# Kernel optimization log

Hardware: AMD Instinct MI355X
Metric: run time of the kernel (lower is better)

The kernel has to match this reference:

```python
import jax, jax.numpy as jnp
import numpy as np

EPS = 1e-6

def _quant_per_token(x):
    # dynamic per-token symmetric int8 quantization (simulated in float)
    s = jnp.max(jnp.abs(x), axis=-1, keepdims=True) / 127.0  # [T,1]
    q = jnp.clip(jnp.round(x / s), -127.0, 127.0)
    return q, s

def _quant_weight(W):
    # per-output-channel symmetric int8 weight quantization (W: [out,in])
    s = jnp.max(jnp.abs(W), axis=1, keepdims=True) / 127.0  # [out,1]
    q = jnp.round(W / s)
    return q, s

def _w8a8(qx, sx, W, b):
    # int8xint8 GEMM with per-token act scale and per-channel weight scale, fp out
    qw, sw = _quant_weight(W)
    return (qx @ qw.T) * (sx * sw.T) + b

def _rmsnorm_bias(x, w, b, eps=EPS):
    # RMSNormGeneral: x * rsqrt(mean(x^2)+eps) * w + b (no mean subtraction)
    var = jnp.mean(x * x, axis=-1, keepdims=True)
    return x * jax.lax.rsqrt(var + eps) * w + b

def setup_inputs() -> dict:
    key = jax.random.key(0)
    ks = jax.random.split(key, 16)
    E, H, F = 1280, 20, 5120
    B, S = 16, 1024
    T = B * S
    d = {
        'hidden': jax.random.normal(ks[0], (T, E), jnp.float32),
        'ln1_w': jax.random.uniform(ks[1], (E,), jnp.float32, 0.5, 1.5),
        'ln1_b': jax.random.normal(ks[2], (E,), jnp.float32) * 0.02,
        'ln2_w': jax.random.uniform(ks[3], (E,), jnp.float32, 0.5, 1.5),
        'ln2_b': jax.random.normal(ks[4], (E,), jnp.float32) * 0.02,
        'W_qkv': jax.random.normal(ks[5], (3 * E, E), jnp.float32) * 0.02,
        'b_qkv': jax.random.normal(ks[6], (3 * E,), jnp.float32) * 0.02,
        'W_out': jax.random.normal(ks[7], (E, E), jnp.float32) * 0.02,
        'b_out': jax.random.normal(ks[8], (E,), jnp.float32) * 0.02,
        'W_fc1': jax.random.normal(ks[9], (F, E), jnp.float32) * 0.02,
        'b_fc1': jax.random.normal(ks[10], (F,), jnp.float32) * 0.02,
        'W_fc2': jax.random.normal(ks[11], (E, F), jnp.float32) * 0.02,
        'b_fc2': jax.random.normal(ks[12], (E,), jnp.float32) * 0.02,
        'bsz': B,
        'seqlen': S,
    }
    return d

def reference(hidden, ln1_w, ln1_b, ln2_w, ln2_b, W_qkv, b_qkv, W_out, b_out,
              W_fc1, b_fc1, W_fc2, b_fc2, bsz, seqlen):
    E = hidden.shape[-1]
    H = 20
    hd = E // H

    # --- self-attention block ---
    residual = hidden
    y = _rmsnorm_bias(hidden, ln1_w, ln1_b)
    qx, sx = _quant_per_token(y)
    qkv = _w8a8(qx, sx, W_qkv, b_qkv)                      # [T, 3E]
    q, k, v = jnp.split(qkv, 3, axis=-1)
    q = q.reshape(bsz, seqlen, H, hd)
    k = k.reshape(bsz, seqlen, H, hd)
    v = v.reshape(bsz, seqlen, H, hd)
    scale = 1.0 / np.sqrt(hd)
    scores = jnp.einsum('bqhd,bkhd->bhqk', q, k) * scale   # non-causal
    probs = jax.nn.softmax(scores, axis=-1)
    attn = jnp.einsum('bhqk,bkhd->bqhd', probs, v).reshape(bsz * seqlen, E)
    qa, sa = _quant_per_token(attn)
    o = _w8a8(qa, sa, W_out, b_out)
    hidden = residual + o

    # --- MLP block ---
    residual = hidden
    y = _rmsnorm_bias(hidden, ln2_w, ln2_b)
    qx, sx = _quant_per_token(y)
    f1 = _w8a8(qx, sx, W_fc1, b_fc1)                       # [T, F]
    g = jax.nn.gelu(f1, approximate=False)                 # fused gelu_and_quant
    qg, sg = _quant_per_token(g)
    f2 = _w8a8(qg, sg, W_fc2, b_fc2)
    return residual + f2
```

## Files before the change

### kernel.cpp

```cpp
#include <hip/hip_runtime.h>
#include <hip/hip_bf16.h>
#include <stdint.h>

#define E_DIM 1280
#define F_DIM 5120
#define T_DIM 16384
#define B_SZ  16
#define S_LEN 1024
#define NH    20

typedef int v4i __attribute__((ext_vector_type(4)));
typedef __attribute__((ext_vector_type(8))) short v8s;
typedef __attribute__((ext_vector_type(4))) float v4f;

__device__ __forceinline__ float wred_sum(float v) {
#pragma unroll
  for (int m = 32; m > 0; m >>= 1) v += __shfl_xor(v, m, 64);
  return v;
}
__device__ __forceinline__ float wred_max(float v) {
#pragma unroll
  for (int m = 32; m > 0; m >>= 1) v = fmaxf(v, __shfl_xor(v, m, 64));
  return v;
}
__device__ __forceinline__ void gload_lds16(const void* g, void* l) {
  __builtin_amdgcn_global_load_lds((const __attribute__((address_space(1))) void*)g,
                                   (__attribute__((address_space(3))) void*)l, 16, 0, 0);
}

__global__ __launch_bounds__(256) void wquant_kernel(
    const float* __restrict__ W, int8_t* __restrict__ qw, float* __restrict__ sw, int K) {
  __shared__ float red[4];
  const int row = blockIdx.x;
  const int tid = threadIdx.x;
  const float* wr = W + (size_t)row * K;
  float amax = 0.f;
  for (int c = tid; c < K; c += 256) amax = fmaxf(amax, fabsf(wr[c]));
  amax = wred_max(amax);
  if ((tid & 63) == 0) red[tid >> 6] = amax;
  __syncthreads();
  amax = fmaxf(fmaxf(red[0], red[1]), fmaxf(red[2], red[3]));
  float sc = amax * (1.0f / 127.0f);
  if (tid == 0) sw[row] = sc;
  for (int c = tid; c < K; c += 256) {
    float qv = rintf(wr[c] / sc);
    qw[(size_t)row * K + c] = (int8_t)qv;
  }
}

__global__ __launch_bounds__(256) void rms_quant_kernel(
    const float* __restrict__ x, const float* __restrict__ w, const float* __restrict__ b,
    int8_t* __restrict__ q, float* __restrict__ s) {
  __shared__ float red[4];
  const int row = blockIdx.x;
  const int tid = threadIdx.x;
  const float* xr = x + (size_t)row * E_DIM;
  float vals[5];
  float ss = 0.f;
#pragma unroll
  for (int i = 0; i < 5; ++i) {
    float v = xr[tid + i * 256];
    vals[i] = v; ss += v * v;
  }
  ss = wred_sum(ss);
  if ((tid & 63) == 0) red[tid >> 6] = ss;
  __syncthreads();
  ss = red[0] + red[1] + red[2] + red[3];
  float rstd = rsqrtf(ss * (1.0f / E_DIM) + 1e-6f);
  float y[5]; float amax = 0.f;
#pragma unroll
  for (int i = 0; i < 5; ++i) {
    int c = tid + i * 256;
    float v = vals[i] * rstd * w[c] + b[c];
    y[i] = v;
    amax = fmaxf(amax, fabsf(v));
  }
  amax = wred_max(amax);
  __syncthreads();
  if ((tid & 63) == 0) red[tid >> 6] = amax;
  __syncthreads();
  amax = fmaxf(fmaxf(red[0], red[1]), fmaxf(red[2], red[3]));
  float sc = amax * (1.0f / 127.0f);
  if (tid == 0) s[row] = sc;
#pragma unroll
  for (int i = 0; i < 5; ++i) {
    int c = tid + i * 256;
    float qv = rintf(y[i] / sc);
    qv = fminf(fmaxf(qv, -127.f), 127.f);
    q[(size_t)row * E_DIM + c] = (int8_t)qv;
  }
}

__global__ __launch_bounds__(256) void row_quant_bf_kernel(
    const __hip_bfloat16* __restrict__ x, int8_t* __restrict__ q, float* __restrict__ s) {
  __shared__ float red[4];
  const int row = blockIdx.x;
  const int tid = threadIdx.x;
  const __hip_bfloat16* xr = x + (size_t)row * E_DIM;
  float vals[5]; float amax = 0.f;
#pragma unroll
  for (int i = 0; i < 5; ++i) {
    float v = __bfloat162float(xr[tid + i * 256]);
    vals[i] = v;
    amax = fmaxf(amax, fabsf(v));
  }
  amax = wred_max(amax);
  if ((tid & 63) == 0) red[tid >> 6] = amax;
  __syncthreads();
  amax = fmaxf(fmaxf(red[0], red[1]), fmaxf(red[2], red[3]));
  float sc = amax * (1.0f / 127.0f);
  if (tid == 0) s[row] = sc;
#pragma unroll
  for (int i = 0; i < 5; ++i) {
    int c = tid + i * 256;
    float qv = rintf(vals[i] / sc);
    qv = fminf(fmaxf(qv, -127.f), 127.f);
    q[(size_t)row * E_DIM + c] = (int8_t)qv;
  }
}

__global__ __launch_bounds__(256) void gelu_quant_kernel(
    const __hip_bfloat16* __restrict__ f1, int8_t* __restrict__ q, float* __restrict__ s) {
  __shared__ float red[4];
  const int row = blockIdx.x;
  const int tid = threadIdx.x;
  const __hip_bfloat16* xr = f1 + (size_t)row * F_DIM;
  float g[20]; float amax = 0.f;
#pragma unroll
  for (int i = 0; i < 20; ++i) {
    float v = __bfloat162float(xr[tid + i * 256]);
    float gv = 0.5f * v * (1.0f + erff(v * 0.70710678118654752440f));
    g[i] = gv;
    amax = fmaxf(amax, fabsf(gv));
  }
  amax = wred_max(amax);
  if ((tid & 63) == 0) red[tid >> 6] = amax;
  __syncthreads();
  amax = fmaxf(fmaxf(red[0], red[1]), fmaxf(red[2], red[3]));
  float sc = amax * (1.0f / 127.0f);
  if (tid == 0) s[row] = sc;
  int8_t* qr = q + (size_t)row * (2 * F_DIM);
#pragma unroll
  for (int i = 0; i < 20; ++i) {
    int c = tid + i * 256;
    float qv = rintf(g[i] / sc);
    qv = fminf(fmaxf(qv, -127.f), 127.f);
    qr[c] = (int8_t)qv;
  }
}

template <int MODE>
__global__ __launch_bounds__(512, 2) void gemm256_i8(
    const int8_t* __restrict__ A, const int8_t* __restrict__ B,
    const float* __restrict__ sx, const float* __restrict__ sw,
    const float* __restrict__ bias, const float* __restrict__ resid,
    void* __restrict__ outp, int M, int N, int K, int lda) {
  __shared__ __align__(16) int8_t As[2][2][256 * 64];
  __shared__ __align__(16) int8_t Bs[2][2][256 * 64];

  const int tid = threadIdx.x;
  const int lane = tid & 63;
  const int wave = tid >> 6;
  const int wm = wave >> 2;
  const int wn = wave & 3;
  const int l16 = lane & 15;
  const int quad = lane >> 4;
  const int choff = (quad ^ ((l16 >> 1) & 3)) << 4;

  const int nwg = gridDim.x;
  const int ntn = N >> 8;
  const int u = (blockIdx.x & 7) * (nwg >> 3) + (blockIdx.x >> 3);
  const int tm = u / ntn, tn = u % ntn;
  const int m0 = tm << 8, n0 = tn << 8;

  const int8_t* A_blk = A + (size_t)m0 * lda;
  const int8_t* B_blk = B + (size_t)n0 * K;

  const int r0 = tid >> 2;
  const int sch = ((tid & 3) ^ ((tid >> 3) & 3)) << 4;

#define STAGE_A(KT, DST)                                                         \
  {                                                                              \
    gload_lds16(A_blk + (size_t)r0 * lda + (size_t)(KT)*64 + sch,                \
                (DST) + tid * 16);                                               \
    gload_lds16(A_blk + (size_t)(r0 + 128) * lda + (size_t)(KT)*64 + sch,        \
                (DST) + 8192 + tid * 16);                                        \
  }
#define STAGE_B(KT, DST)                                                         \
  {                                                                              \
    gload_lds16(B_blk + (size_t)r0 * K + (size_t)(KT)*64 + sch,                  \
                (DST) + tid * 16);                                               \
    gload_lds16(B_blk + (size_t)(r0 + 128) * K + (size_t)(KT)*64 + sch,          \
                (DST) + 8192 + tid * 16);                                        \
  }

  v4i acc[8][4];
#pragma unroll
  for (int i = 0; i < 8; ++i)
#pragma unroll
    for (int j = 0; j < 4; ++j) acc[i][j] = (v4i){0, 0, 0, 0};

  const int nk = K >> 6;
  const int niter = nk >> 1;

  STAGE_A(0, &As[0][0][0]); STAGE_B(0, &Bs[0][0][0]);
  STAGE_A(1, &As[0][1][0]); STAGE_B(1, &Bs[0][1][0]);
  asm volatile("s_waitcnt vmcnt(4)" ::: "memory");
  asm volatile("s_barrier" ::: "memory");

#pragma unroll 1
  for (int i = 0; i < niter - 1; ++i) {
    const int pr = i & 1;
    const int kt2 = 2 * i + 2;
#pragma unroll
    for (int ph = 0; ph < 4; ++ph) {
      const int tt = ph >> 1;
      const int qm = ph & 1;
      const int8_t* At = &As[pr][tt][0];
      const int8_t* Bt = &Bs[pr][tt][0];
      v4i af[4], bf[4];
#pragma unroll
      for (int ii = 0; ii < 4; ++ii)
        af[ii] = *(const v4i*)(At + (wm * 128 + qm * 64 + ii * 16 + l16) * 64 + choff);
#pragma unroll
      for (int jj = 0; jj < 4; ++jj)
        bf[jj] = *(const v4i*)(Bt + (wn * 64 + jj * 16 + l16) * 64 + choff);
      if (qm == 0) {
        STAGE_A(kt2 + tt, &As[pr ^ 1][tt][0]);
      } else {
        STAGE_B(kt2 + tt, &Bs[pr ^ 1][tt][0]);
      }
      asm volatile("s_barrier" ::: "memory");
      __builtin_amdgcn_s_setprio(1);
#pragma unroll
      for (int ii = 0; ii < 4; ++ii)
#pragma unroll
        for (int jj = 0; jj < 4; ++jj)
          acc[qm * 4 + ii][jj] = __builtin_amdgcn_mfma_i32_16x16x64_i8(
              af[ii], bf[jj], acc[qm * 4 + ii][jj], 0, 0, 0);
      __builtin_amdgcn_s_setprio(0);
      if (qm == 1) asm volatile("s_waitcnt vmcnt(4)" ::: "memory");
      asm volatile("s_barrier" ::: "memory");
    }
  }

  {
    const int pr = (niter - 1) & 1;
#pragma unroll
    for (int ph = 0; ph < 4; ++ph) {
      const int tt = ph >> 1;
      const int qm = ph & 1;
      const int8_t* At = &As[pr][tt][0];
      const int8_t* Bt = &Bs[pr][tt][0];
      v4i af[4], bf[4];
#pragma unroll
      for (int ii = 0; ii < 4; ++ii)
        af[ii] = *(const v4i*)(At + (wm * 128 + qm * 64 + ii * 16 + l16) * 64 + choff);
#pragma unroll
      for (int jj = 0; jj < 4; ++jj)
        bf[jj] = *(const v4i*)(Bt + (wn * 64 + jj * 16 + l16) * 64 + choff);
      asm volatile("s_barrier" ::: "memory");
      __builtin_amdgcn_s_setprio(1);
#pragma unroll
      for (int ii = 0; ii < 4; ++ii)
#pragma unroll
        for (int jj = 0; jj < 4; ++jj)
          acc[qm * 4 + ii][jj] = __builtin_amdgcn_mfma_i32_16x16x64_i8(
              af[ii], bf[jj], acc[qm * 4 + ii][jj], 0, 0, 0);
      __builtin_amdgcn_s_setprio(0);
      if (ph == 1) asm volatile("s_waitcnt vmcnt(0)" ::: "memory");
      asm volatile("s_barrier" ::: "memory");
    }
  }
#undef STAGE_A
#undef STAGE_B

  float swv[4], bv[4];
#pragma unroll
  for (int jj = 0; jj < 4; ++jj) {
    int n = n0 + wn * 64 + jj * 16 + l16;
    swv[jj] = sw[n];
    bv[jj] = bias[n];
  }
#pragma unroll
  for (int mf = 0; mf < 8; ++mf) {
#pragma unroll
    for (int r = 0; r < 4; ++r) {
      int m = m0 + wm * 128 + mf * 16 + quad * 4 + r;
      float sxm = sx[m];
#pragma unroll
      for (int jj = 0; jj < 4; ++jj) {
        int n = n0 + wn * 64 + jj * 16 + l16;
        float v = (float)acc[mf][jj][r] * (sxm * swv[jj]) + bv[jj];
        if constexpr (MODE == 0) {
          ((__hip_bfloat16*)outp)[(size_t)m * N + n] = __float2bfloat16(v);
        } else {
          ((float*)outp)[(size_t)m * N + n] = v + resid[(size_t)m * N + n];
        }
      }
    }
  }
}

__global__ __launch_bounds__(256) void vt_kernel(
    const __hip_bfloat16* __restrict__ qkv, __hip_bfloat16* __restrict__ Vt) {
  __shared__ __hip_bfloat16 tile[64][72];
  const int bh = blockIdx.y, kc = blockIdx.x;
  const int b = bh / NH, h = bh % NH;
  const int tid = threadIdx.x;
  const size_t base = ((size_t)b * S_LEN + (size_t)kc * 64) * (3 * E_DIM) + 2 * E_DIM + h * 64;
#pragma unroll
  for (int i = 0; i < 2; ++i) {
    int idx = tid + i * 256;
    int row = idx >> 3, c8 = (idx & 7) * 8;
    *(uint4*)&tile[row][c8] = *(const uint4*)(qkv + base + (size_t)row * (3 * E_DIM) + c8);
  }
  __syncthreads();
#pragma unroll
  for (int i = 0; i < 2; ++i) {
    int idx = tid + i * 256;
    int d = idx >> 3, k8 = (idx & 7) * 8;
    __hip_bfloat16 v[8] __attribute__((aligned(16)));
#pragma unroll
    for (int j = 0; j < 8; ++j) v[j] = tile[k8 + j][d];
    *(uint4*)&Vt[((size_t)bh * 64 + d) * 1024 + (size_t)kc * 64 + k8] = *(uint4*)v;
  }
}

__global__ __launch_bounds__(256) void attn_flash_kernel(
    const __hip_bfloat16* __restrict__ qkv, const __hip_bfloat16* __restrict__ Vt,
    __hip_bfloat16* __restrict__ attn) {
  constexpr int E3 = 3 * E_DIM;
  __shared__ __align__(16) __hip_bfloat16 Ks[128 * 64];
  __shared__ __align__(16) __hip_bfloat16 Vs[64 * 128];
  __shared__ __align__(16) __hip_bfloat16 Ps[4][16 * 128];
  __shared__ float stats[4][16];

  const int tid = threadIdx.x;
  const int lane = tid & 63;
  const int wave = tid >> 6;
  const int l16 = lane & 15;
  const int quad = lane >> 4;
  const int bh = blockIdx.y;
  const int b = bh / NH, h = bh % NH;
  const int q0 = blockIdx.x * 64;
  const size_t base_t = (size_t)b * S_LEN;

  v8s qb0, qb1;
  {
    const __hip_bfloat16* qp =
        qkv + (base_t + q0 + wave * 16 + l16) * (size_t)E3 + h * 64 + quad * 8;
    qb0 = *(const v8s*)qp;
    qb1 = *(const v8s*)(qp + 32);
  }

  float m_prev = -3.0e38f;
  float lsum = 0.f;
  v4f oc[4];
#pragma unroll
  for (int dt = 0; dt < 4; ++dt) oc[dt] = (v4f){0.f, 0.f, 0.f, 0.f};

  const __hip_bfloat16* kgbase = qkv + base_t * E3 + E_DIM + h * 64;
  const __hip_bfloat16* vgbase = Vt + (size_t)bh * 64 * 1024;
  __hip_bfloat16* pw = Ps[wave];

#pragma unroll 1
  for (int t = 0; t < 8; ++t) {
    __syncthreads();
#pragma unroll
    for (int i = 0; i < 4; ++i) {
      int c = tid + i * 256;
      int row = c >> 3, lc = c & 7;
      int gc = lc ^ (row & 7);
      gload_lds16(kgbase + (size_t)(t * 128 + row) * E3 + gc * 8, (char*)Ks + c * 16);
    }
#pragma unroll
    for (int i = 0; i < 4; ++i) {
      int c = tid + i * 256;
      int d = c >> 4, lc = c & 15;
      int gc = lc ^ (d & 15);
      gload_lds16(vgbase + (size_t)d * 1024 + t * 128 + gc * 8, (char*)Vs + c * 16);
    }
    __syncthreads();

    v4f accT[8];
#pragma unroll
    for (int nt = 0; nt < 8; ++nt) {
      int row = nt * 16 + l16;
      const char* kr = (const char*)Ks + row * 128;
      v8s ak0 = *(const v8s*)(kr + ((quad ^ (row & 7)) * 16));
      v8s ak1 = *(const v8s*)(kr + (((quad + 4) ^ (row & 7)) * 16));
      v4f z = {0.f, 0.f, 0.f, 0.f};
      z = __builtin_amdgcn_mfma_f32_16x16x32_bf16(ak0, qb0, z, 0, 0, 0);
      accT[nt] = __builtin_amdgcn_mfma_f32_16x16x32_bf16(ak1, qb1, accT[nt] = z, 0, 0, 0);
    }

    float mt = -3.0e38f;
#pragma unroll
    for (int nt = 0; nt < 8; ++nt)
#pragma unroll
      for (int r = 0; r < 4; ++r) mt = fmaxf(mt, accT[nt][r]);
    mt = fmaxf(mt, __shfl_xor(mt, 16, 64));
    mt = fmaxf(mt, __shfl_xor(mt, 32, 64));
    float m_new = fmaxf(m_prev, mt);
    float alpha = __expf(0.125f * (m_prev - m_new));
    m_prev = m_new;
    float ts = 0.f;
#pragma unroll
    for (int nt = 0; nt < 8; ++nt)
#pragma unroll
      for (int r = 0; r < 4; ++r) {
        float e = __expf(0.125f * (accT[nt][r] - m_new));
        accT[nt][r] = e;
        ts += e;
      }
    lsum = lsum * alpha + ts;
    if (quad == 0) stats[wave][l16] = alpha;
#pragma unroll
    for (int nt = 0; nt < 8; ++nt) {
      __hip_bfloat16 pk[4] __attribute__((aligned(8)));
#pragma unroll
      for (int r = 0; r < 4; ++r) pk[r] = __float2bfloat16(accT[nt][r]);
      int lcq = 2 * nt + (quad >> 1);
      *(uint2*)((char*)pw + l16 * 256 + ((lcq ^ l16) * 16) + (quad & 1) * 8) = *(uint2*)pk;
    }
    v4f a4 = *(v4f*)&stats[wave][quad * 4];
#pragma unroll
    for (int dt = 0; dt < 4; ++dt)
#pragma unroll
      for (int r = 0; r < 4; ++r) oc[dt][r] *= a4[r];
#pragma unroll
    for (int ks = 0; ks < 4; ++ks) {
      int pch = (ks * 4 + quad) ^ l16;
      v8s ap = *(const v8s*)((char*)pw + l16 * 256 + pch * 16);
#pragma unroll
      for (int dt = 0; dt < 4; ++dt) {
        int d = dt * 16 + l16;
        v8s bv = *(const v8s*)((char*)Vs + d * 256 + (((ks * 4 + quad) ^ l16) * 16));
        oc[dt] = __builtin_amdgcn_mfma_f32_16x16x32_bf16(ap, bv, oc[dt], 0, 0, 0);
      }
    }
  }

  lsum += __shfl_xor(lsum, 16, 64);
  lsum += __shfl_xor(lsum, 32, 64);
  if (quad == 0) stats[wave][l16] = lsum;
  v4f l4 = *(v4f*)&stats[wave][quad * 4];
  float inv[4];
#pragma unroll
  for (int r = 0; r < 4; ++r) inv[r] = 1.0f / l4[r];
#pragma unroll
  for (int dt = 0; dt < 4; ++dt)
#pragma unroll
    for (int r = 0; r < 4; ++r) {
      int tok = q0 + wave * 16 + quad * 4 + r;
      attn[(base_t + tok) * (size_t)E_DIM + h * 64 + dt * 16 + l16] =
          __float2bfloat16(oc[dt][r] * inv[r]);
    }
}

extern "C" void kernel_launch(void* const* d_in, const int* in_sizes, int n_in,
                              void* d_out, int out_size, void* d_ws, size_t ws_size,
                              hipStream_t stream) {
  const float* hidden = (const float*)d_in[0];
  const float* ln1_w = (const float*)d_in[1];
  const float* ln1_b = (const float*)d_in[2];
  const float* ln2_w = (const float*)d_in[3];
  const float* ln2_b = (const float*)d_in[4];
  const float* W_qkv = (const float*)d_in[5];
  const float* b_qkv = (const float*)d_in[6];
  const float* W_out = (const float*)d_in[7];
  const float* b_out = (const float*)d_in[8];
  const float* W_fc1 = (const float*)d_in[9];
  const float* b_fc1 = (const float*)d_in[10];
  const float* W_fc2 = (const float*)d_in[11];
  const float* b_fc2 = (const float*)d_in[12];

  char* ws = (char*)d_ws;
  size_t off = 0;
  auto alloc = [&](size_t bytes) {
    void* p = ws + off;
    off += (bytes + 255) & ~(size_t)255;
    return p;
  };
  int8_t* qw_qkv = (int8_t*)alloc((size_t)3 * E_DIM * E_DIM);
  int8_t* qw_out = (int8_t*)alloc((size_t)E_DIM * E_DIM);
  int8_t* qw_fc1 = (int8_t*)alloc((size_t)F_DIM * E_DIM);
  int8_t* qw_fc2 = (int8_t*)alloc((size_t)E_DIM * F_DIM);
  float* sw_qkv = (float*)alloc((size_t)3 * E_DIM * 4);
  float* sw_out = (float*)alloc((size_t)E_DIM * 4);
  float* sw_fc1 = (float*)alloc((size_t)F_DIM * 4);
  float* sw_fc2 = (float*)alloc((size_t)E_DIM * 4);
  float* sx1 = (float*)alloc((size_t)T_DIM * 4);
  float* sa  = (float*)alloc((size_t)T_DIM * 4);
  float* sx2 = (float*)alloc((size_t)T_DIM * 4);
  float* sg  = (float*)alloc((size_t)T_DIM * 4);
  int8_t* qx = (int8_t*)alloc((size_t)T_DIM * E_DIM);
  char* R = (char*)alloc((size_t)T_DIM * 3 * E_DIM * 2 +
                         (size_t)T_DIM * E_DIM * 4);
  __hip_bfloat16* qkv_bf = (__hip_bfloat16*)R;
  __hip_bfloat16* attn_bf = (__hip_bfloat16*)(R + (size_t)T_DIM * 3 * E_DIM * 2);
  __hip_bfloat16* Vt = (__hip_bfloat16*)(R + (size_t)T_DIM * 3 * E_DIM * 2 +
                                         (size_t)T_DIM * E_DIM * 2);
  __hip_bfloat16* f1_bf = (__hip_bfloat16*)R;
  int8_t* qg = (int8_t*)R;
  float* hidden2 = (float*)d_out;

  wquant_kernel<<<3 * E_DIM, 256, 0, stream>>>(W_qkv, qw_qkv, sw_qkv, E_DIM);
  wquant_kernel<<<E_DIM, 256, 0, stream>>>(W_out, qw_out, sw_out, E_DIM);
  wquant_kernel<<<F_DIM, 256, 0, stream>>>(W_fc1, qw_fc1, sw_fc1, E_DIM);
  wquant_kernel<<<E_DIM, 256, 0, stream>>>(W_fc2, qw_fc2, sw_fc2, F_DIM);
  rms_quant_kernel<<<T_DIM, 256, 0, stream>>>(hidden, ln1_w, ln1_b, qx, sx1);
  gemm256_i8<0><<<(T_DIM / 256) * (3 * E_DIM / 256), 512, 0, stream>>>(
      qx, qw_qkv, sx1, sw_qkv, b_qkv, nullptr, qkv_bf, T_DIM, 3 * E_DIM, E_DIM, E_DIM);
  vt_kernel<<<dim3(S_LEN / 64, B_SZ * NH), 256, 0, stream>>>(qkv_bf, Vt);
  attn_flash_kernel<<<dim3(S_LEN / 64, B_SZ * NH), 256, 0, stream>>>(qkv_bf, Vt, attn_bf);
  row_quant_bf_kernel<<<T_DIM, 256, 0, stream>>>(attn_bf, qx, sa);
  gemm256_i8<1><<<(T_DIM / 256) * (E_DIM / 256), 512, 0, stream>>>(
      qx, qw_out, sa, sw_out, b_out, hidden, hidden2, T_DIM, E_DIM, E_DIM, E_DIM);
  rms_quant_kernel<<<T_DIM, 256, 0, stream>>>(hidden2, ln2_w, ln2_b, qx, sx2);
  gemm256_i8<0><<<(T_DIM / 256) * (F_DIM / 256), 512, 0, stream>>>(
      qx, qw_fc1, sx2, sw_fc1, b_fc1, nullptr, f1_bf, T_DIM, F_DIM, E_DIM, E_DIM);
  gelu_quant_kernel<<<T_DIM, 256, 0, stream>>>(f1_bf, qg, sg);
  gemm256_i8<1><<<(T_DIM / 256) * (E_DIM / 256), 512, 0, stream>>>(
      qg, qw_fc2, sg, sw_fc2, b_fc2, hidden2, (float*)d_out, T_DIM, E_DIM, F_DIM, 2 * F_DIM);
}
```

Before: 1.136 ms.

## Switch GEMMs to 32x32x32 int8 MFMA and add 128-tile kernel for narrow GEMMs

Replaces the 16x16x64 int8 MFMA fragments in the 256-tile GEMM with 32x32x32 MFMAs. This changes the LDS fragment indexing and the epilogue row mapping. It also adds a 128x128-tile, 4-wave GEMM with a 4-slot LDS ring for the two N=1280 GEMMs (out-proj and fc2), so more workgroups run and the GPU fills better on the narrow outputs. The risks are more LDS passes per FLOP on the smaller tile, and getting the swizzle and output mapping right.

```diff
diff --git a/kernel.cpp b/kernel.cpp
--- a/kernel.cpp
+++ b/kernel.cpp
@@ -10,6 +10,7 @@
 #define NH    20
 
 typedef int v4i __attribute__((ext_vector_type(4)));
+typedef int v16i __attribute__((ext_vector_type(16)));
 typedef __attribute__((ext_vector_type(8))) short v8s;
 typedef __attribute__((ext_vector_type(4))) float v4f;
 
@@ -163,9 +164,11 @@
   const int wave = tid >> 6;
   const int wm = wave >> 2;
   const int wn = wave & 3;
-  const int l16 = lane & 15;
-  const int quad = lane >> 4;
-  const int choff = (quad ^ ((l16 >> 1) & 3)) << 4;
+  const int l32 = lane & 31;
+  const int h = lane >> 5;
+  const int swz = (l32 >> 1) & 3;
+  const int ch0 = ((0 + h) ^ swz) << 4;
+  const int ch1 = ((2 + h) ^ swz) << 4;
 
   const int nwg = gridDim.x;
   const int ntn = N >> 8;
@@ -194,11 +197,11 @@
                 (DST) + 8192 + tid * 16);                                        \
   }
 
-  v4i acc[8][4];
-#pragma unroll
-  for (int i = 0; i < 8; ++i)
-#pragma unroll
-    for (int j = 0; j < 4; ++j) acc[i][j] = (v4i){0, 0, 0, 0};
+  v16i acc[4][2];
+#pragma unroll
+  for (int i = 0; i < 4; ++i)
+#pragma unroll
+    for (int j = 0; j < 2; ++j) acc[i][j] = (v16i)(0);
 
   const int nk = K >> 6;
   const int niter = nk >> 1;
@@ -215,17 +218,18 @@
 #pragma unroll
     for (int ph = 0; ph < 4; ++ph) {
       const int tt = ph >> 1;
-      const int qm = ph & 1;
+      const int s = ph & 1;
       const int8_t* At = &As[pr][tt][0];
       const int8_t* Bt = &Bs[pr][tt][0];
-      v4i af[4], bf[4];
-#pragma unroll
-      for (int ii = 0; ii < 4; ++ii)
-        af[ii] = *(const v4i*)(At + (wm * 128 + qm * 64 + ii * 16 + l16) * 64 + choff);
-#pragma unroll
-      for (int jj = 0; jj < 4; ++jj)
-        bf[jj] = *(const v4i*)(Bt + (wn * 64 + jj * 16 + l16) * 64 + choff);
-      if (qm == 0) {
+      const int ch = s ? ch1 : ch0;
+      v4i af[4], bf[2];
+#pragma unroll
+      for (int mf = 0; mf < 4; ++mf)
+        af[mf] = *(const v4i*)(At + (wm * 128 + mf * 32 + l32) * 64 + ch);
+#pragma unroll
+      for (int nf = 0; nf < 2; ++nf)
+        bf[nf] = *(const v4i*)(Bt + (wn * 64 + nf * 32 + l32) * 64 + ch);
+      if (s == 0) {
         STAGE_A(kt2 + tt, &As[pr ^ 1][tt][0]);
       } else {
         STAGE_B(kt2 + tt, &Bs[pr ^ 1][tt][0]);
@@ -233,13 +237,13 @@
       asm volatile("s_barrier" ::: "memory");
       __builtin_amdgcn_s_setprio(1);
 #pragma unroll
-      for (int ii = 0; ii < 4; ++ii)
-#pragma unroll
-        for (int jj = 0; jj < 4; ++jj)
-          acc[qm * 4 + ii][jj] = __builtin_amdgcn_mfma_i32_16x16x64_i8(
-              af[ii], bf[jj], acc[qm * 4 + ii][jj], 0, 0, 0);
+      for (int mf = 0; mf < 4; ++mf)
+#pragma unroll
+        for (int nf = 0; nf < 2; ++nf)
+          acc[mf][nf] = __builtin_amdgcn_mfma_i32_32x32x32_i8(
+              af[mf], bf[nf], acc[mf][nf], 0, 0, 0);
       __builtin_amdgcn_s_setprio(0);
-      if (qm == 1) asm volatile("s_waitcnt vmcnt(4)" ::: "memory");
+      if (s == 1) asm volatile("s_waitcnt vmcnt(4)" ::: "memory");
       asm volatile("s_barrier" ::: "memory");
     }
   }
@@ -249,24 +253,25 @@
 #pragma unroll
     for (int ph = 0; ph < 4; ++ph) {
       const int tt = ph >> 1;
-      const int qm = ph & 1;
+      const int s = ph & 1;
       const int8_t* At = &As[pr][tt][0];
       const int8_t* Bt = &Bs[pr][tt][0];
-      v4i af[4], bf[4];
-#pragma unroll
-      for (int ii = 0; ii < 4; ++ii)
-        af[ii] = *(const v4i*)(At + (wm * 128 + qm * 64 + ii * 16 + l16) * 64 + choff);
-#pragma unroll
-      for (int jj = 0; jj < 4; ++jj)
-        bf[jj] = *(const v4i*)(Bt + (wn * 64 + jj * 16 + l16) * 64 + choff);
+      const int ch = s ? ch1 : ch0;
+      v4i af[4], bf[2];
+#pragma unroll
+      for (int mf = 0; mf < 4; ++mf)
+        af[mf] = *(const v4i*)(At + (wm * 128 + mf * 32 + l32) * 64 + ch);
+#pragma unroll
+      for (int nf = 0; nf < 2; ++nf)
+        bf[nf] = *(const v4i*)(Bt + (wn * 64 + nf * 32 + l32) * 64 + ch);
       asm volatile("s_barrier" ::: "memory");
       __builtin_amdgcn_s_setprio(1);
 #pragma unroll
-      for (int ii = 0; ii < 4; ++ii)
-#pragma unroll
-        for (int jj = 0; jj < 4; ++jj)
-          acc[qm * 4 + ii][jj] = __builtin_amdgcn_mfma_i32_16x16x64_i8(
-              af[ii], bf[jj], acc[qm * 4 + ii][jj], 0, 0, 0);
+      for (int mf = 0; mf < 4; ++mf)
+#pragma unroll
+        for (int nf = 0; nf < 2; ++nf)
+          acc[mf][nf] = __builtin_amdgcn_mfma_i32_32x32x32_i8(
+              af[mf], bf[nf], acc[mf][nf], 0, 0, 0);
       __builtin_amdgcn_s_setprio(0);
       if (ph == 1) asm volatile("s_waitcnt vmcnt(0)" ::: "memory");
       asm volatile("s_barrier" ::: "memory");
@@ -275,23 +280,154 @@
 #undef STAGE_A
 #undef STAGE_B
 
-  float swv[4], bv[4];
-#pragma unroll
-  for (int jj = 0; jj < 4; ++jj) {
-    int n = n0 + wn * 64 + jj * 16 + l16;
-    swv[jj] = sw[n];
-    bv[jj] = bias[n];
-  }
-#pragma unroll
-  for (int mf = 0; mf < 8; ++mf) {
-#pragma unroll
-    for (int r = 0; r < 4; ++r) {
-      int m = m0 + wm * 128 + mf * 16 + quad * 4 + r;
+  float swv[2], bv[2];
+#pragma unroll
+  for (int nf = 0; nf < 2; ++nf) {
+    int n = n0 + wn * 64 + nf * 32 + l32;
+    swv[nf] = sw[n];
+    bv[nf] = bias[n];
+  }
+#pragma unroll
+  for (int mf = 0; mf < 4; ++mf) {
+    const int mbase = m0 + wm * 128 + mf * 32 + 4 * h;
+#pragma unroll
+    for (int r = 0; r < 16; ++r) {
+      int m = mbase + (r & 3) + 8 * (r >> 2);
       float sxm = sx[m];
 #pragma unroll
-      for (int jj = 0; jj < 4; ++jj) {
-        int n = n0 + wn * 64 + jj * 16 + l16;
-        float v = (float)acc[mf][jj][r] * (sxm * swv[jj]) + bv[jj];
+      for (int nf = 0; nf < 2; ++nf) {
+        int n = n0 + wn * 64 + nf * 32 + l32;
+        float v = (float)acc[mf][nf][r] * (sxm * swv[nf]) + bv[nf];
+        if constexpr (MODE == 0) {
+          ((__hip_bfloat16*)outp)[(size_t)m * N + n] = __float2bfloat16(v);
+        } else {
+          ((float*)outp)[(size_t)m * N + n] = v + resid[(size_t)m * N + n];
+        }
+      }
+    }
+  }
+}
+
+template <int MODE>
+__global__ __launch_bounds__(256, 2) void gemm128_i8(
+    const int8_t* __restrict__ A, const int8_t* __restrict__ B,
+    const float* __restrict__ sx, const float* __restrict__ sw,
+    const float* __restrict__ bias, const float* __restrict__ resid,
+    void* __restrict__ outp, int M, int N, int K, int lda) {
+  __shared__ __align__(16) int8_t As[4][128 * 64];
+  __shared__ __align__(16) int8_t Bs[4][128 * 64];
+
+  const int tid = threadIdx.x;
+  const int lane = tid & 63;
+  const int wave = tid >> 6;
+  const int wm = wave >> 1;
+  const int wn = wave & 1;
+  const int l32 = lane & 31;
+  const int h = lane >> 5;
+  const int swz = (l32 >> 1) & 3;
+  const int ch0 = ((0 + h) ^ swz) << 4;
+  const int ch1 = ((2 + h) ^ swz) << 4;
+
+  const int nwg = gridDim.x;
+  const int ntn = N >> 7;
+  const int u = (blockIdx.x & 7) * (nwg >> 3) + (blockIdx.x >> 3);
+  const int tm = u / ntn, tn = u % ntn;
+  const int m0 = tm << 7, n0 = tn << 7;
+
+  const int8_t* A_blk = A + (size_t)m0 * lda;
+  const int8_t* B_blk = B + (size_t)n0 * K;
+
+  const int r0 = tid >> 2;
+  const int sch = ((tid & 3) ^ ((tid >> 3) & 3)) << 4;
+
+#define STAGE_A(KT, SLOT)                                                        \
+  {                                                                              \
+    gload_lds16(A_blk + (size_t)r0 * lda + (size_t)(KT)*64 + sch,                \
+                &As[SLOT][tid * 16]);                                            \
+    gload_lds16(A_blk + (size_t)(r0 + 64) * lda + (size_t)(KT)*64 + sch,         \
+                &As[SLOT][4096 + tid * 16]);                                     \
+  }
+#define STAGE_B(KT, SLOT)                                                        \
+  {                                                                              \
+    gload_lds16(B_blk + (size_t)r0 * K + (size_t)(KT)*64 + sch,                  \
+                &Bs[SLOT][tid * 16]);                                            \
+    gload_lds16(B_blk + (size_t)(r0 + 64) * K + (size_t)(KT)*64 + sch,           \
+                &Bs[SLOT][4096 + tid * 16]);                                     \
+  }
+
+#define PHASE128(SLOT, CH, STAGE_STMT, WAIT_STMT)                                \
+  {                                                                              \
+    const int8_t* At = &As[SLOT][0];                                             \
+    const int8_t* Bt = &Bs[SLOT][0];                                             \
+    v4i af[2], bf[2];                                                            \
+    _Pragma("unroll") for (int mf = 0; mf < 2; ++mf)                             \
+        af[mf] = *(const v4i*)(At + (wm * 64 + mf * 32 + l32) * 64 + (CH));      \
+    _Pragma("unroll") for (int nf = 0; nf < 2; ++nf)                             \
+        bf[nf] = *(const v4i*)(Bt + (wn * 64 + nf * 32 + l32) * 64 + (CH));      \
+    STAGE_STMT;                                                                  \
+    asm volatile("s_barrier" ::: "memory");                                      \
+    __builtin_amdgcn_s_setprio(1);                                               \
+    _Pragma("unroll") for (int mf = 0; mf < 2; ++mf)                             \
+        _Pragma("unroll") for (int nf = 0; nf < 2; ++nf)                         \
+            acc[mf][nf] = __builtin_amdgcn_mfma_i32_32x32x32_i8(                 \
+                af[mf], bf[nf], acc[mf][nf], 0, 0, 0);                           \
+    __builtin_amdgcn_s_setprio(0);                                               \
+    WAIT_STMT;                                                                   \
+    asm volatile("s_barrier" ::: "memory");                                      \
+  }
+
+  v16i acc[2][2];
+#pragma unroll
+  for (int i = 0; i < 2; ++i)
+#pragma unroll
+    for (int j = 0; j < 2; ++j) acc[i][j] = (v16i)(0);
+
+  const int nk = K >> 6;
+
+  STAGE_A(0, 0); STAGE_B(0, 0);
+  STAGE_A(1, 1); STAGE_B(1, 1);
+  STAGE_A(2, 2); STAGE_B(2, 2);
+  asm volatile("s_waitcnt vmcnt(8)" ::: "memory");
+  asm volatile("s_barrier" ::: "memory");
+
+#pragma unroll 1
+  for (int kt = 0; kt < nk - 3; ++kt) {
+    const int sl = kt & 3;
+    const int s3 = (kt + 3) & 3;
+    PHASE128(sl, ch0, STAGE_A(kt + 3, s3), ((void)0));
+    PHASE128(sl, ch1, STAGE_B(kt + 3, s3),
+             asm volatile("s_waitcnt vmcnt(8)" ::: "memory"));
+  }
+  PHASE128((nk - 3) & 3, ch0, ((void)0), ((void)0));
+  PHASE128((nk - 3) & 3, ch1, ((void)0),
+           asm volatile("s_waitcnt vmcnt(4)" ::: "memory"));
+  PHASE128((nk - 2) & 3, ch0, ((void)0), ((void)0));
+  PHASE128((nk - 2) & 3, ch1, ((void)0),
+           asm volatile("s_waitcnt vmcnt(0)" ::: "memory"));
+  PHASE128((nk - 1) & 3, ch0, ((void)0), ((void)0));
+  PHASE128((nk - 1) & 3, ch1, ((void)0), ((void)0));
+#undef PHASE128
+#undef STAGE_A
+#undef STAGE_B
+
+  float swv[2], bv[2];
+#pragma unroll
+  for (int nf = 0; nf < 2; ++nf) {
+    int n = n0 + wn * 64 + nf * 32 + l32;
+    swv[nf] = sw[n];
+    bv[nf] = bias[n];
+  }
+#pragma unroll
+  for (int mf = 0; mf < 2; ++mf) {
+    const int mbase = m0 + wm * 64 + mf * 32 + 4 * h;
+#pragma unroll
+    for (int r = 0; r < 16; ++r) {
+      int m = mbase + (r & 3) + 8 * (r >> 2);
+      float sxm = sx[m];
+#pragma unroll
+      for (int nf = 0; nf < 2; ++nf) {
+        int n = n0 + wn * 64 + nf * 32 + l32;
+        float v = (float)acc[mf][nf][r] * (sxm * swv[nf]) + bv[nf];
         if constexpr (MODE == 0) {
           ((__hip_bfloat16*)outp)[(size_t)m * N + n] = __float2bfloat16(v);
         } else {
@@ -516,12 +652,12 @@
   vt_kernel<<<dim3(S_LEN / 64, B_SZ * NH), 256, 0, stream>>>(qkv_bf, Vt);
   attn_flash_kernel<<<dim3(S_LEN / 64, B_SZ * NH), 256, 0, stream>>>(qkv_bf, Vt, attn_bf);
   row_quant_bf_kernel<<<T_DIM, 256, 0, stream>>>(attn_bf, qx, sa);
-  gemm256_i8<1><<<(T_DIM / 256) * (E_DIM / 256), 512, 0, stream>>>(
+  gemm128_i8<1><<<(T_DIM / 128) * (E_DIM / 128), 256, 0, stream>>>(
       qx, qw_out, sa, sw_out, b_out, hidden, hidden2, T_DIM, E_DIM, E_DIM, E_DIM);
   rms_quant_kernel<<<T_DIM, 256, 0, stream>>>(hidden2, ln2_w, ln2_b, qx, sx2);
   gemm256_i8<0><<<(T_DIM / 256) * (F_DIM / 256), 512, 0, stream>>>(
       qx, qw_fc1, sx2, sw_fc1, b_fc1, nullptr, f1_bf, T_DIM, F_DIM, E_DIM, E_DIM);
   gelu_quant_kernel<<<T_DIM, 256, 0, stream>>>(f1_bf, qg, sg);
-  gemm256_i8<1><<<(T_DIM / 256) * (E_DIM / 256), 512, 0, stream>>>(
+  gemm128_i8<1><<<(T_DIM / 128) * (E_DIM / 128), 256, 0, stream>>>(
       qg, qw_fc2, sg, sw_fc2, b_fc2, hidden2, (float*)d_out, T_DIM, E_DIM, F_DIM, 2 * F_DIM);
 }
```

Result: faster. 1.085 ms (-4.5%).

## Merge GEMM k-phases into full 256-row tiles; shrink attention P buffer for occupancy

Applied to the files above, without the earlier changes.

The int8 GEMM main loop now processes each 64-wide k-tile as one 8x4 MFMA block per wave with a single A+B stage issue, halving barriers per k-tile at the cost of holding more A fragments in registers. The flash attention kernel writes P to LDS in 32-column chunks interleaved with the PV MFMAs, shrinking the per-wave P buffer fourfold. It also adds a launch bound of 4 blocks per CU to raise occupancy. Risks include register pressure or spills in the GEMM, and extra LDS round-trips in attention.

```diff
diff --git a/kernel.cpp b/kernel.cpp
--- a/kernel.cpp
+++ b/kernel.cpp
@@ -194,6 +194,27 @@
                 (DST) + 8192 + tid * 16);                                        \
   }
 
+#define KTILE256(PR, TT, STAGE_STMT, WAIT_STMT)                                  \
+  {                                                                              \
+    const int8_t* At = &As[PR][TT][0];                                           \
+    const int8_t* Bt = &Bs[PR][TT][0];                                           \
+    v4i af[8], bf[4];                                                            \
+    _Pragma("unroll") for (int ii = 0; ii < 8; ++ii)                             \
+        af[ii] = *(const v4i*)(At + (wm * 128 + ii * 16 + l16) * 64 + choff);    \
+    _Pragma("unroll") for (int jj = 0; jj < 4; ++jj)                             \
+        bf[jj] = *(const v4i*)(Bt + (wn * 64 + jj * 16 + l16) * 64 + choff);     \
+    STAGE_STMT;                                                                  \
+    asm volatile("s_barrier" ::: "memory");                                      \
+    __builtin_amdgcn_s_setprio(1);                                               \
+    _Pragma("unroll") for (int ii = 0; ii < 8; ++ii)                             \
+        _Pragma("unroll") for (int jj = 0; jj < 4; ++jj)                         \
+            acc[ii][jj] = __builtin_amdgcn_mfma_i32_16x16x64_i8(                 \
+                af[ii], bf[jj], acc[ii][jj], 0, 0, 0);                           \
+    __builtin_amdgcn_s_setprio(0);                                               \
+    WAIT_STMT;                                                                   \
+    asm volatile("s_barrier" ::: "memory");                                      \
+  }
+
   v4i acc[8][4];
 #pragma unroll
   for (int i = 0; i < 8; ++i)
@@ -212,66 +233,20 @@
   for (int i = 0; i < niter - 1; ++i) {
     const int pr = i & 1;
     const int kt2 = 2 * i + 2;
-#pragma unroll
-    for (int ph = 0; ph < 4; ++ph) {
-      const int tt = ph >> 1;
-      const int qm = ph & 1;
-      const int8_t* At = &As[pr][tt][0];
-      const int8_t* Bt = &Bs[pr][tt][0];
-      v4i af[4], bf[4];
-#pragma unroll
-      for (int ii = 0; ii < 4; ++ii)
-        af[ii] = *(const v4i*)(At + (wm * 128 + qm * 64 + ii * 16 + l16) * 64 + choff);
-#pragma unroll
-      for (int jj = 0; jj < 4; ++jj)
-        bf[jj] = *(const v4i*)(Bt + (wn * 64 + jj * 16 + l16) * 64 + choff);
-      if (qm == 0) {
-        STAGE_A(kt2 + tt, &As[pr ^ 1][tt][0]);
-      } else {
-        STAGE_B(kt2 + tt, &Bs[pr ^ 1][tt][0]);
-      }
-      asm volatile("s_barrier" ::: "memory");
-      __builtin_amdgcn_s_setprio(1);
-#pragma unroll
-      for (int ii = 0; ii < 4; ++ii)
-#pragma unroll
-        for (int jj = 0; jj < 4; ++jj)
-          acc[qm * 4 + ii][jj] = __builtin_amdgcn_mfma_i32_16x16x64_i8(
-              af[ii], bf[jj], acc[qm * 4 + ii][jj], 0, 0, 0);
-      __builtin_amdgcn_s_setprio(0);
-      if (qm == 1) asm volatile("s_waitcnt vmcnt(4)" ::: "memory");
-      asm volatile("s_barrier" ::: "memory");
-    }
+    KTILE256(pr, 0,
+             { STAGE_A(kt2, &As[pr ^ 1][0][0]); STAGE_B(kt2, &Bs[pr ^ 1][0][0]); },
+             asm volatile("s_waitcnt vmcnt(4)" ::: "memory"));
+    KTILE256(pr, 1,
+             { STAGE_A(kt2 + 1, &As[pr ^ 1][1][0]); STAGE_B(kt2 + 1, &Bs[pr ^ 1][1][0]); },
+             asm volatile("s_waitcnt vmcnt(4)" ::: "memory"));
   }
 
   {
     const int pr = (niter - 1) & 1;
-#pragma unroll
-    for (int ph = 0; ph < 4; ++ph) {
-      const int tt = ph >> 1;
-      const int qm = ph & 1;
-      const int8_t* At = &As[pr][tt][0];
-      const int8_t* Bt = &Bs[pr][tt][0];
-      v4i af[4], bf[4];
-#pragma unroll
-      for (int ii = 0; ii < 4; ++ii)
-        af[ii] = *(const v4i*)(At + (wm * 128 + qm * 64 + ii * 16 + l16) * 64 + choff);
-#pragma unroll
-      for (int jj = 0; jj < 4; ++jj)
-        bf[jj] = *(const v4i*)(Bt + (wn * 64 + jj * 16 + l16) * 64 + choff);
-      asm volatile("s_barrier" ::: "memory");
-      __builtin_amdgcn_s_setprio(1);
-#pragma unroll
-      for (int ii = 0; ii < 4; ++ii)
-#pragma unroll
-        for (int jj = 0; jj < 4; ++jj)
-          acc[qm * 4 + ii][jj] = __builtin_amdgcn_mfma_i32_16x16x64_i8(
-              af[ii], bf[jj], acc[qm * 4 + ii][jj], 0, 0, 0);
-      __builtin_amdgcn_s_setprio(0);
-      if (ph == 1) asm volatile("s_waitcnt vmcnt(0)" ::: "memory");
-      asm volatile("s_barrier" ::: "memory");
-    }
-  }
+    KTILE256(pr, 0, ((void)0), asm volatile("s_waitcnt vmcnt(0)" ::: "memory"));
+    KTILE256(pr, 1, ((void)0), ((void)0));
+  }
+#undef KTILE256
 #undef STAGE_A
 #undef STAGE_B
 
@@ -327,13 +302,13 @@
   }
 }
 
-__global__ __launch_bounds__(256) void attn_flash_kernel(
+__global__ __launch_bounds__(256, 4) void attn_flash_kernel(
     const __hip_bfloat16* __restrict__ qkv, const __hip_bfloat16* __restrict__ Vt,
     __hip_bfloat16* __restrict__ attn) {
   constexpr int E3 = 3 * E_DIM;
   __shared__ __align__(16) __hip_bfloat16 Ks[128 * 64];
   __shared__ __align__(16) __hip_bfloat16 Vs[64 * 128];
-  __shared__ __align__(16) __hip_bfloat16 Ps[4][16 * 128];
+  __shared__ __align__(16) __hip_bfloat16 Ps[4][16 * 32];
   __shared__ float stats[4][16];
 
   const int tid = threadIdx.x;
@@ -362,7 +337,8 @@
 
   const __hip_bfloat16* kgbase = qkv + base_t * E3 + E_DIM + h * 64;
   const __hip_bfloat16* vgbase = Vt + (size_t)bh * 64 * 1024;
-  __hip_bfloat16* pw = Ps[wave];
+  char* pw = (char*)Ps[wave];
+  const int pswz = (l16 >> 1) & 3;
 
 #pragma unroll 1
   for (int t = 0; t < 8; ++t) {
@@ -416,27 +392,28 @@
       }
     lsum = lsum * alpha + ts;
     if (quad == 0) stats[wave][l16] = alpha;
-#pragma unroll
-    for (int nt = 0; nt < 8; ++nt) {
-      __hip_bfloat16 pk[4] __attribute__((aligned(8)));
-#pragma unroll
-      for (int r = 0; r < 4; ++r) pk[r] = __float2bfloat16(accT[nt][r]);
-      int lcq = 2 * nt + (quad >> 1);
-      *(uint2*)((char*)pw + l16 * 256 + ((lcq ^ l16) * 16) + (quad & 1) * 8) = *(uint2*)pk;
-    }
     v4f a4 = *(v4f*)&stats[wave][quad * 4];
 #pragma unroll
     for (int dt = 0; dt < 4; ++dt)
 #pragma unroll
       for (int r = 0; r < 4; ++r) oc[dt][r] *= a4[r];
-#pragma unroll
-    for (int ks = 0; ks < 4; ++ks) {
-      int pch = (ks * 4 + quad) ^ l16;
-      v8s ap = *(const v8s*)((char*)pw + l16 * 256 + pch * 16);
+
+#pragma unroll
+    for (int j = 0; j < 4; ++j) {
+#pragma unroll
+      for (int e2 = 0; e2 < 2; ++e2) {
+        int nt = 2 * j + e2;
+        __hip_bfloat16 pk[4] __attribute__((aligned(8)));
+#pragma unroll
+        for (int r = 0; r < 4; ++r) pk[r] = __float2bfloat16(accT[nt][r]);
+        int lcw = 2 * e2 + (quad >> 1);
+        *(uint2*)(pw + l16 * 64 + ((lcw ^ pswz) * 16) + (quad & 1) * 8) = *(uint2*)pk;
+      }
+      v8s ap = *(const v8s*)(pw + l16 * 64 + ((quad ^ pswz) * 16));
 #pragma unroll
       for (int dt = 0; dt < 4; ++dt) {
         int d = dt * 16 + l16;
-        v8s bv = *(const v8s*)((char*)Vs + d * 256 + (((ks * 4 + quad) ^ l16) * 16));
+        v8s bv = *(const v8s*)((char*)Vs + d * 256 + (((j * 4 + quad) ^ l16) * 16));
         oc[dt] = __builtin_amdgcn_mfma_f32_16x16x32_bf16(ap, bv, oc[dt], 0, 0, 0);
       }
     }
```

Measured after the change: 1.080 ms. 4.9% less time.
